# Performance work log

Measured on AMD Instinct MI355X. Metric: run time of the kernel, lower is better.

The kernel has to match this reference:

```python
import jax, jax.numpy as jnp
import numpy as np

N_ATOMS = 100_000
N_PAIRS = 6_400_000
N_BATCH = 16


def smooth_switch(x, x0, x1):
    t = (x - x0) / (x1 - x0)
    tc = jnp.clip(t, 1e-9, 1.0 - 1e-9)  # safe interior values
    f1 = jnp.exp(-1.0 / tc)
    f2 = jnp.exp(-1.0 / (1.0 - tc))
    s = f1 / (f1 + f2)
    return jnp.where(t <= 0.0, 0.0, jnp.where(t >= 1.0, 1.0, s))


def setup_inputs() -> dict:
    key = jax.random.key(0)
    k1, k2, k3, k4, k5 = jax.random.split(key, 5)
    atomic_numbers = jax.random.randint(k1, (N_ATOMS,), 1, 81).astype(jnp.float32)
    # displacements scaled so distances span the (0, 10) switch window
    displacements = jax.random.normal(k2, (N_PAIRS, 3), dtype=jnp.float32) * 2.5
    idx_i = jnp.sort(jax.random.randint(k3, (N_PAIRS,), 0, N_ATOMS)).astype(jnp.int32)
    idx_j = jax.random.randint(k4, (N_PAIRS,), 0, N_ATOMS).astype(jnp.int32)
    atom_mask = jnp.ones((N_ATOMS,), dtype=jnp.float32)
    batch_mask = jnp.ones((N_PAIRS,), dtype=jnp.float32)
    batch_segments = jnp.sort(jax.random.randint(k5, (N_ATOMS,), 0, N_BATCH)).astype(jnp.int32)
    # ZBL parameters (non-trainable constants in the module)
    a_coefficient = jnp.asarray(0.8854, dtype=jnp.float32)
    a_exponent = jnp.asarray(0.23, dtype=jnp.float32)
    phi_coefficients = jnp.asarray([0.18175, 0.50986, 0.28022, 0.02817], dtype=jnp.float32)
    phi_exponents = jnp.asarray([3.1998, 0.94229, 0.4029, 0.20162], dtype=jnp.float32)
    return {
        "atomic_numbers": atomic_numbers,
        "displacements": displacements,
        "idx_i": idx_i,
        "idx_j": idx_j,
        "atom_mask": atom_mask,
        "batch_mask": batch_mask,
        "batch_segments": batch_segments,
        "batch_size": N_BATCH,
        "a_coefficient": a_coefficient,
        "a_exponent": a_exponent,
        "phi_coefficients": phi_coefficients,
        "phi_exponents": phi_exponents,
    }


def reference(atomic_numbers, displacements, idx_i, idx_j, atom_mask, batch_mask,
              batch_segments, batch_size, a_coefficient, a_exponent,
              phi_coefficients, phi_exponents):
    n_atoms = atomic_numbers.shape[0]
    displacements = displacements + (1.0 - batch_mask[..., None])
    distances = jnp.maximum(jnp.linalg.norm(displacements, axis=-1), 1e-10)  # [P]
    switch_off = smooth_switch(distances, 0.0, 10.0)

    safe_atomic_numbers = jnp.maximum(atomic_numbers, 1e-06)
    za = jnp.exp(jnp.log(safe_atomic_numbers) * jnp.abs(a_exponent))
    za = jnp.nan_to_num(za, nan=1e-06, posinf=1e6, neginf=1e-06)
    za_sum = za[idx_i] + za[idx_j]                     # [P]
    denominator = jnp.maximum(za_sum, 1e-06)
    a_ij = jnp.abs(a_coefficient) / denominator
    a_ij = jnp.nan_to_num(a_ij, nan=1e-06, posinf=1e6, neginf=1e-06)
    arguments = jnp.maximum(distances, 1e-10) / jnp.maximum(a_ij, 1e-10)
    arguments = jnp.nan_to_num(arguments, nan=1e-06, posinf=1e6, neginf=1e-06)

    raw_coefficients = jnp.abs(phi_coefficients)
    coefficients = raw_coefficients / jnp.maximum(jnp.sum(raw_coefficients), 1e-10)
    exponents = jnp.maximum(jnp.abs(phi_exponents), 1e-10)
    log_terms = -exponents[None, :] * arguments[:, None]          # [P,4]
    max_log = jnp.max(log_terms, axis=1, keepdims=True)           # [P,1]
    exp_terms = jnp.exp(log_terms - max_log)
    exp_terms = jnp.nan_to_num(exp_terms, nan=0.0, posinf=1.0, neginf=0.0)
    phi = jnp.sum(coefficients[None, :] * exp_terms, axis=1) * jnp.exp(max_log)[..., 0]
    phi = jnp.maximum(phi, 1e-30)
    phi = jnp.nan_to_num(phi, nan=1e-30, posinf=1e6, neginf=1e-30)

    safe_distances = jnp.maximum(distances, 1e-10)
    safe_phi = jnp.maximum(phi, 1e-30)
    safe_switch = jnp.maximum(switch_off, 1e-30)
    charge_product = jnp.minimum(safe_atomic_numbers[idx_i] * safe_atomic_numbers[idx_j], 1e4)
    base_repulsion = jnp.minimum(0.5 * charge_product / safe_distances, 1e6)
    repulsion = base_repulsion * safe_phi * safe_switch
    repulsion = jnp.clip(repulsion, 0.0, 1e6)
    repulsion = jnp.nan_to_num(repulsion, nan=0.0, posinf=1e6, neginf=0.0)
    repulsion = repulsion * batch_mask

    Erep = jax.ops.segment_sum(repulsion, segment_ids=idx_i, num_segments=n_atoms)
    Erep = Erep * atom_mask
    Erep = jnp.clip(Erep, 0.0, 1e6)
    Erep = jnp.nan_to_num(Erep, nan=0.0, posinf=1e6, neginf=0.0)
    Erep = Erep * 0.01
    return Erep[..., None, None, None]  # [N,1,1,1]
```

## Files before the change

kernel.cpp:

```cpp
#include <hip/hip_runtime.h>
#include <math.h>


#define LOG2E 1.4426950408889634f

static __device__ __forceinline__ float rcpf_(float x)  { return __builtin_amdgcn_rcpf(x); }
static __device__ __forceinline__ float exp2f_(float x) { return __builtin_amdgcn_exp2f(x); }
static __device__ __forceinline__ float sqrtf_(float x) { return __builtin_amdgcn_sqrtf(x); }
static __device__ __forceinline__ float expn_(float x)  { return exp2f_(x * LOG2E); }

__global__ void zbl_setup_tab(const float* __restrict__ an,
                              const float* __restrict__ a_exp_ptr,
                              float2* __restrict__ tab, int n) {
    int i = blockIdx.x * blockDim.x + threadIdx.x;
    if (i >= n) return;
    float ae = fabsf(a_exp_ptr[0]);
    float sa = fmaxf(an[i], 1e-6f);
    float z  = expf(logf(sa) * ae);
    if (!(z == z)) z = 1e-6f;
    z = fminf(z, 1e6f);
    tab[i] = make_float2(z, sa);
}

__global__ __launch_bounds__(256) void zbl_pair_kernel(
    const float* __restrict__ disp,
    const int*   __restrict__ idx_i,
    const int*   __restrict__ idx_j,
    const float* __restrict__ batch_mask,
    const float2* __restrict__ tab,
    const float* __restrict__ a_coef_ptr,
    const float* __restrict__ phi_c,
    const float* __restrict__ phi_e,
    float* __restrict__ out_acc,
    int nP)
{
    __shared__ float sdisp[256 * 3];
    const int tid  = threadIdx.x;
    const int base = blockIdx.x * 256;

    {
        long gbase = (long)base * 3;
        long total = (long)nP * 3;
        if (tid < 192) {
            long g = gbase + (long)tid * 4;
            if (g + 3 < total) {
                float4 v = *reinterpret_cast<const float4*>(disp + g);
                reinterpret_cast<float4*>(sdisp)[tid] = v;
            } else {
                #pragma unroll
                for (int k = 0; k < 4; ++k)
                    sdisp[tid * 4 + k] = (g + k < total) ? disp[g + k] : 0.0f;
            }
        }
    }
    __syncthreads();

    const int p = base + tid;
    float rep = 0.0f;
    int   key = -1;

    if (p < nP) {
        float bm  = batch_mask[p];
        float add = 1.0f - bm;
        float dx = sdisp[tid * 3 + 0] + add;
        float dy = sdisp[tid * 3 + 1] + add;
        float dz = sdisp[tid * 3 + 2] + add;
        float dist = fmaxf(sqrtf_(dx * dx + dy * dy + dz * dz), 1e-10f);

        float t  = dist * 0.1f;
        float tc = fminf(fmaxf(t, 1e-9f), 1.0f - 1e-9f);
        float u  = rcpf_(tc) - rcpf_(1.0f - tc);
        float s  = rcpf_(1.0f + expn_(u));
        float sw = (t <= 0.0f) ? 0.0f : ((t >= 1.0f) ? 1.0f : s);

        int ii = idx_i[p];
        int jj = idx_j[p];
        float2 ti = tab[ii];
        float2 tj = tab[jj];

        float za_sum = ti.x + tj.x;
        float arg = fminf(dist * za_sum * rcpf_(fmaxf(fabsf(a_coef_ptr[0]), 1e-10f)), 1e6f);

        float c0 = fabsf(phi_c[0]), c1 = fabsf(phi_c[1]);
        float c2 = fabsf(phi_c[2]), c3 = fabsf(phi_c[3]);
        float cinv = rcpf_(fmaxf(c0 + c1 + c2 + c3, 1e-10f));
        float narg = -arg * LOG2E;
        float e0 = fmaxf(fabsf(phi_e[0]), 1e-10f);
        float e1 = fmaxf(fabsf(phi_e[1]), 1e-10f);
        float e2 = fmaxf(fabsf(phi_e[2]), 1e-10f);
        float e3 = fmaxf(fabsf(phi_e[3]), 1e-10f);
        float phi = (c0 * exp2f_(e0 * narg) + c1 * exp2f_(e1 * narg) +
                     c2 * exp2f_(e2 * narg) + c3 * exp2f_(e3 * narg)) * cinv;
        phi = fminf(fmaxf(phi, 1e-30f), 1e6f);

        float cp   = fminf(ti.y * tj.y, 1e4f);
        float brep = fminf(0.5f * cp * rcpf_(dist), 1e6f);
        float r    = brep * phi * fmaxf(sw, 1e-30f);
        r = fminf(fmaxf(r, 0.0f), 1e6f);
        if (!(r == r)) r = 0.0f;
        rep = r * bm;
        key = ii;
    }

    const int lane = tid & 63;
    float v = rep;
    #pragma unroll
    for (int d = 1; d < 64; d <<= 1) {
        float nv = __shfl_down(v, d);
        int   nk = __shfl_down(key, d);
        if (lane + d < 64 && nk == key) v += nv;
    }
    int pk = __shfl_up(key, 1);
    bool head = (lane == 0) || (pk != key);
    if (head && key >= 0) {
        atomicAdd(&out_acc[key], v);
    }
}

__global__ void zbl_epilogue(float* __restrict__ out,
                             const float* __restrict__ atom_mask, int n) {
    int i = blockIdx.x * blockDim.x + threadIdx.x;
    if (i >= n) return;
    float v = out[i] * atom_mask[i];
    v = fminf(fmaxf(v, 0.0f), 1e6f);
    if (!(v == v)) v = 0.0f;
    out[i] = v * 0.01f;
}

extern "C" void kernel_launch(void* const* d_in, const int* in_sizes, int n_in,
                              void* d_out, int out_size, void* d_ws, size_t ws_size,
                              hipStream_t stream) {
    const float* an         = (const float*)d_in[0];
    const float* disp       = (const float*)d_in[1];
    const int*   idx_i      = (const int*)d_in[2];
    const int*   idx_j      = (const int*)d_in[3];
    const float* atom_mask  = (const float*)d_in[4];
    const float* batch_mask = (const float*)d_in[5];
    const float* a_coef     = (const float*)d_in[8];
    const float* a_exp      = (const float*)d_in[9];
    const float* phi_c      = (const float*)d_in[10];
    const float* phi_e      = (const float*)d_in[11];

    const int nA = in_sizes[0];
    const int nP = in_sizes[2];
    float* out = (float*)d_out;

    hipMemsetAsync(d_out, 0, (size_t)out_size * sizeof(float), stream);

    float2* tab = (float2*)d_ws;

    zbl_setup_tab<<<(nA + 255) / 256, 256, 0, stream>>>(an, a_exp, tab, nA);
    zbl_pair_kernel<<<(nP + 255) / 256, 256, 0, stream>>>(
        disp, idx_i, idx_j, batch_mask, tab, a_coef, phi_c, phi_e, out, nP);
    zbl_epilogue<<<(nA + 255) / 256, 256, 0, stream>>>(out, atom_mask, nA);
}
```

Measured before the change: 55.04 us.

## Process four pairs per thread with vector loads and run-length pre-reduction

Each thread now handles four consecutive pairs, loading indices, masks and displacements with float4/int4 vector loads instead of staging displacements through shared memory. Sorted idx_i runs are summed in registers before the wavefront segmented shuffle reduction. Parameter preprocessing is hoisted per thread, and the switch and distance math use rsqrt and a fused reciprocal. This launches a quarter as many threads, which reduces occupancy and latency hiding for the random gathers into tab. It also adds a small atomic when a run ends inside a thread's four pairs.

```diff
diff --git a/kernel.cpp b/kernel.cpp
--- a/kernel.cpp
+++ b/kernel.cpp
@@ -5,9 +5,8 @@
 #define LOG2E 1.4426950408889634f
 
 static __device__ __forceinline__ float rcpf_(float x)  { return __builtin_amdgcn_rcpf(x); }
+static __device__ __forceinline__ float rsqf_(float x)  { return __builtin_amdgcn_rsqf(x); }
 static __device__ __forceinline__ float exp2f_(float x) { return __builtin_amdgcn_exp2f(x); }
-static __device__ __forceinline__ float sqrtf_(float x) { return __builtin_amdgcn_sqrtf(x); }
-static __device__ __forceinline__ float expn_(float x)  { return exp2f_(x * LOG2E); }
 
 __global__ void zbl_setup_tab(const float* __restrict__ an,
                               const float* __restrict__ a_exp_ptr,
@@ -22,6 +21,36 @@
     tab[i] = make_float2(z, sa);
 }
 
+static __device__ __forceinline__ float pair_rep(
+    float dx, float dy, float dz, float bm, float2 ti, float2 tj,
+    float ac_inv, float c0, float c1, float c2, float c3,
+    float e0, float e1, float e2, float e3)
+{
+    float d2   = fmaxf(dx * dx + dy * dy + dz * dz, 1e-20f);
+    float rsq  = rsqf_(d2);
+    float dist = d2 * rsq;
+
+    float tt = dist * 0.1f;
+    float tc = fminf(fmaxf(tt, 1e-9f), 1.0f - 1e-9f);
+    float u  = (1.0f - 2.0f * tc) * rcpf_(tc - tc * tc);
+    float s  = rcpf_(1.0f + exp2f_(u * LOG2E));
+    float sw = (tt >= 1.0f) ? 1.0f : s;
+
+    float za_sum = ti.x + tj.x;
+    float arg  = fminf(dist * za_sum * ac_inv, 1e6f);
+    float narg = -arg * LOG2E;
+    float phi  = c0 * exp2f_(e0 * narg) + c1 * exp2f_(e1 * narg) +
+                 c2 * exp2f_(e2 * narg) + c3 * exp2f_(e3 * narg);
+    phi = fminf(fmaxf(phi, 1e-30f), 1e6f);
+
+    float cp   = fminf(ti.y * tj.y, 1e4f);
+    float brep = fminf(0.5f * cp * rsq, 1e6f);
+    float r    = brep * phi * fmaxf(sw, 1e-30f);
+    r = fminf(fmaxf(r, 0.0f), 1e6f);
+    if (!(r == r)) r = 0.0f;
+    return r * bm;
+}
+
 __global__ __launch_bounds__(256) void zbl_pair_kernel(
     const float* __restrict__ disp,
     const int*   __restrict__ idx_i,
@@ -34,76 +63,78 @@
     float* __restrict__ out_acc,
     int nP)
 {
-    __shared__ float sdisp[256 * 3];
-    const int tid  = threadIdx.x;
-    const int base = blockIdx.x * 256;
+    const int t  = blockIdx.x * 256 + threadIdx.x;
+    const int p0 = t * 4;
 
-    {
-        long gbase = (long)base * 3;
-        long total = (long)nP * 3;
-        if (tid < 192) {
-            long g = gbase + (long)tid * 4;
-            if (g + 3 < total) {
-                float4 v = *reinterpret_cast<const float4*>(disp + g);
-                reinterpret_cast<float4*>(sdisp)[tid] = v;
+    const float ac_inv = rcpf_(fmaxf(fabsf(a_coef_ptr[0]), 1e-10f));
+    float c0 = fabsf(phi_c[0]), c1 = fabsf(phi_c[1]);
+    float c2 = fabsf(phi_c[2]), c3 = fabsf(phi_c[3]);
+    const float cinv = rcpf_(fmaxf(c0 + c1 + c2 + c3, 1e-10f));
+    c0 *= cinv; c1 *= cinv; c2 *= cinv; c3 *= cinv;
+    const float e0 = fmaxf(fabsf(phi_e[0]), 1e-10f);
+    const float e1 = fmaxf(fabsf(phi_e[1]), 1e-10f);
+    const float e2 = fmaxf(fabsf(phi_e[2]), 1e-10f);
+    const float e3 = fmaxf(fabsf(phi_e[3]), 1e-10f);
+
+    float runsum = 0.0f;
+    int   runkey = -1;
+
+    if (p0 + 3 < nP) {
+        const int4   ii4 = *reinterpret_cast<const int4*>(idx_i + p0);
+        const int4   jj4 = *reinterpret_cast<const int4*>(idx_j + p0);
+        const float4 bm4 = *reinterpret_cast<const float4*>(batch_mask + p0);
+        const long   g   = (long)p0 * 3;
+        const float4 da  = *reinterpret_cast<const float4*>(disp + g);
+        const float4 db  = *reinterpret_cast<const float4*>(disp + g + 4);
+        const float4 dc  = *reinterpret_cast<const float4*>(disp + g + 8);
+
+        const int   ii[4] = {ii4.x, ii4.y, ii4.z, ii4.w};
+        const int   jj[4] = {jj4.x, jj4.y, jj4.z, jj4.w};
+        const float bm[4] = {bm4.x, bm4.y, bm4.z, bm4.w};
+        const float dx[4] = {da.x, da.w, db.z, dc.y};
+        const float dy[4] = {da.y, db.x, db.w, dc.z};
+        const float dz[4] = {da.z, db.y, dc.x, dc.w};
+
+        #pragma unroll
+        for (int k = 0; k < 4; ++k) {
+            float add = 1.0f - bm[k];
+            float2 ti = tab[ii[k]];
+            float2 tj = tab[jj[k]];
+            float rep = pair_rep(dx[k] + add, dy[k] + add, dz[k] + add, bm[k],
+                                 ti, tj, ac_inv, c0, c1, c2, c3, e0, e1, e2, e3);
+            if (ii[k] == runkey) {
+                runsum += rep;
             } else {
-                #pragma unroll
-                for (int k = 0; k < 4; ++k)
-                    sdisp[tid * 4 + k] = (g + k < total) ? disp[g + k] : 0.0f;
+                if (runkey >= 0) atomicAdd(&out_acc[runkey], runsum);
+                runkey = ii[k];
+                runsum = rep;
+            }
+        }
+    } else if (p0 < nP) {
+        for (int k = 0; k < 4; ++k) {
+            int p = p0 + k;
+            if (p >= nP) break;
+            float bmv = batch_mask[p];
+            float add = 1.0f - bmv;
+            int ik = idx_i[p], jk = idx_j[p];
+            float2 ti = tab[ik];
+            float2 tj = tab[jk];
+            long g = (long)p * 3;
+            float rep = pair_rep(disp[g] + add, disp[g + 1] + add, disp[g + 2] + add,
+                                 bmv, ti, tj, ac_inv, c0, c1, c2, c3, e0, e1, e2, e3);
+            if (ik == runkey) {
+                runsum += rep;
+            } else {
+                if (runkey >= 0) atomicAdd(&out_acc[runkey], runsum);
+                runkey = ik;
+                runsum = rep;
             }
         }
     }
-    __syncthreads();
 
-    const int p = base + tid;
-    float rep = 0.0f;
-    int   key = -1;
-
-    if (p < nP) {
-        float bm  = batch_mask[p];
-        float add = 1.0f - bm;
-        float dx = sdisp[tid * 3 + 0] + add;
-        float dy = sdisp[tid * 3 + 1] + add;
-        float dz = sdisp[tid * 3 + 2] + add;
-        float dist = fmaxf(sqrtf_(dx * dx + dy * dy + dz * dz), 1e-10f);
-
-        float t  = dist * 0.1f;
-        float tc = fminf(fmaxf(t, 1e-9f), 1.0f - 1e-9f);
-        float u  = rcpf_(tc) - rcpf_(1.0f - tc);
-        float s  = rcpf_(1.0f + expn_(u));
-        float sw = (t <= 0.0f) ? 0.0f : ((t >= 1.0f) ? 1.0f : s);
-
-        int ii = idx_i[p];
-        int jj = idx_j[p];
-        float2 ti = tab[ii];
-        float2 tj = tab[jj];
-
-        float za_sum = ti.x + tj.x;
-        float arg = fminf(dist * za_sum * rcpf_(fmaxf(fabsf(a_coef_ptr[0]), 1e-10f)), 1e6f);
-
-        float c0 = fabsf(phi_c[0]), c1 = fabsf(phi_c[1]);
-        float c2 = fabsf(phi_c[2]), c3 = fabsf(phi_c[3]);
-        float cinv = rcpf_(fmaxf(c0 + c1 + c2 + c3, 1e-10f));
-        float narg = -arg * LOG2E;
-        float e0 = fmaxf(fabsf(phi_e[0]), 1e-10f);
-        float e1 = fmaxf(fabsf(phi_e[1]), 1e-10f);
-        float e2 = fmaxf(fabsf(phi_e[2]), 1e-10f);
-        float e3 = fmaxf(fabsf(phi_e[3]), 1e-10f);
-        float phi = (c0 * exp2f_(e0 * narg) + c1 * exp2f_(e1 * narg) +
-                     c2 * exp2f_(e2 * narg) + c3 * exp2f_(e3 * narg)) * cinv;
-        phi = fminf(fmaxf(phi, 1e-30f), 1e6f);
-
-        float cp   = fminf(ti.y * tj.y, 1e4f);
-        float brep = fminf(0.5f * cp * rcpf_(dist), 1e6f);
-        float r    = brep * phi * fmaxf(sw, 1e-30f);
-        r = fminf(fmaxf(r, 0.0f), 1e6f);
-        if (!(r == r)) r = 0.0f;
-        rep = r * bm;
-        key = ii;
-    }
-
-    const int lane = tid & 63;
-    float v = rep;
+    const int lane = threadIdx.x & 63;
+    float v = runsum;
+    int   key = runkey;
     #pragma unroll
     for (int d = 1; d < 64; d <<= 1) {
         float nv = __shfl_down(v, d);
@@ -150,7 +181,8 @@
     float2* tab = (float2*)d_ws;
 
     zbl_setup_tab<<<(nA + 255) / 256, 256, 0, stream>>>(an, a_exp, tab, nA);
-    zbl_pair_kernel<<<(nP + 255) / 256, 256, 0, stream>>>(
+    const int threads_needed = (nP + 3) / 4;
+    zbl_pair_kernel<<<(threads_needed + 255) / 256, 256, 0, stream>>>(
         disp, idx_i, idx_j, batch_mask, tab, a_coef, phi_c, phi_e, out, nP);
     zbl_epilogue<<<(nA + 255) / 256, 256, 0, stream>>>(out, atom_mask, nA);
 }
```

New measurement: 58.30 us. 5.9% more time.
